# Kernel tuning notes

Measured on AMD Instinct MI355X. Metric: run time of the kernel, lower is better.

Reference implementation:

```python
import jax, jax.numpy as jnp
import numpy as np

N = 50000
F_IN = 256
H1, D1 = 8, 8            # conv1: 8 heads x 8 dims, concat -> 64
H2, C = 8, 16            # conv2: 8 heads x num_classes, concat -> 128
NEG_SLOPE = 0.2


def setup_inputs() -> dict:
    key = jax.random.key(0)
    ks = jax.random.split(key, 10)
    x = jax.random.normal(ks[0], (N, F_IN), dtype=jnp.float32)
    edge_index = jax.random.randint(ks[1], (2, 800000), 0, N, dtype=jnp.int64)
    s1 = 1.0 / np.sqrt(F_IN)
    s2 = 1.0 / np.sqrt(H1 * D1)
    return {
        "x": x,
        "edge_index": edge_index,
        "W1": jax.random.normal(ks[2], (F_IN, H1 * D1), dtype=jnp.float32) * s1,
        "a1_src": jax.random.normal(ks[3], (H1, D1), dtype=jnp.float32) * s2,
        "a1_dst": jax.random.normal(ks[4], (H1, D1), dtype=jnp.float32) * s2,
        "b1": jnp.zeros((H1 * D1,), dtype=jnp.float32),
        "W2": jax.random.normal(ks[5], (H1 * D1, H2 * C), dtype=jnp.float32) * s2,
        "a2_src": jax.random.normal(ks[6], (H2, C), dtype=jnp.float32) * (1.0 / np.sqrt(C)),
        "a2_dst": jax.random.normal(ks[7], (H2, C), dtype=jnp.float32) * (1.0 / np.sqrt(C)),
        "b2": jnp.zeros((H2 * C,), dtype=jnp.float32),
    }


def _add_self_loops(edge_index, n):
    loops = jnp.arange(n, dtype=edge_index.dtype)
    return jnp.concatenate([edge_index, jnp.stack([loops, loops])], axis=1)


def _gat_conv(x, src, dst, W, a_src, a_dst, b, heads, out_dim, n):
    # xw: [N, H, O]
    xw = (x @ W).reshape(n, heads, out_dim)
    al_src = jnp.einsum("nho,ho->nh", xw, a_src)  # [N, H]
    al_dst = jnp.einsum("nho,ho->nh", xw, a_dst)
    e = jax.nn.leaky_relu(al_src[src] + al_dst[dst], NEG_SLOPE)  # [E, H]
    # segment softmax over edges sharing a destination node
    e_max = jax.ops.segment_max(e, dst, num_segments=n)
    e_exp = jnp.exp(e - e_max[dst])
    denom = jax.ops.segment_sum(e_exp, dst, num_segments=n)
    alpha = e_exp / (denom[dst] + 1e-16)                          # [E, H]
    msg = xw[src] * alpha[:, :, None]                              # [E, H, O]
    out = jax.ops.segment_sum(msg, dst, num_segments=n)           # [N, H, O]
    return out.reshape(n, heads * out_dim) + b, alpha


def reference(x, edge_index, W1, a1_src, a1_dst, b1, W2, a2_src, a2_dst, b2):
    ei = _add_self_loops(edge_index, N)
    src, dst = ei[0], ei[1]
    # dropout is a no-op at inference (training=False)
    h1, alpha1 = _gat_conv(x, src, dst, W1, a1_src, a1_dst, b1, H1, D1, N)
    h1 = jax.nn.elu(h1)
    h2, _ = _gat_conv(h1, src, dst, W2, a2_src, a2_dst, b2, H2, C, N)
    logp = jax.nn.log_softmax(h2, axis=1)
    return logp, alpha1
```

## Files before the change

### kernel.cpp

```cpp
#include <hip/hip_runtime.h>

#define N_NODES 50000
#define N_EDGES 800000
#define N_TOT   850000
#define NEG 0.2f
#define ELLW 64

#define G1_TILES 782
#define G2_TILES 782

#define NBIN   250
#define NPBIN  200
#define BKBLK  200
#define EPBK   4000
#define BCAP   32
#define OCAP   4096

__device__ __forceinline__ float leaky(float x) { return x > 0.f ? x : NEG * x; }

__device__ __forceinline__ unsigned bf16pk(float a, float b) {
  unsigned ua = __float_as_uint(a), ub = __float_as_uint(b);
  ua = (ua + 0x7FFFu + ((ua >> 16) & 1u)) >> 16;
  ub = (ub + 0x7FFFu + ((ub >> 16) & 1u)) >> 16;
  return ua | (ub << 16);
}
__device__ __forceinline__ float blo(unsigned u) { return __uint_as_float(u << 16); }
__device__ __forceinline__ float bhi(unsigned u) { return __uint_as_float(u & 0xFFFF0000u); }
__device__ __forceinline__ float bh2f(unsigned short h) { return __uint_as_float(((unsigned)h) << 16); }

__global__ __launch_bounds__(256) void bin_gemm1_k(const float* __restrict__ x,
    const float* __restrict__ W1, const float* __restrict__ a1sv, const float* __restrict__ a1dv,
    unsigned short* __restrict__ xw1h, float* __restrict__ al1s, float* __restrict__ a1dd,
    const int* __restrict__ srcA, const int* __restrict__ dstA,
    unsigned* __restrict__ slots, unsigned short* __restrict__ bcnt2,
    unsigned* __restrict__ ofl, int* __restrict__ ofc)
{
  __shared__ __align__(16) char smem[33024];
  const int t = threadIdx.x;
  if (blockIdx.x < BKBLK) {
    unsigned (*buf)[BCAP] = (unsigned(*)[BCAP])smem;
    int* bc = (int*)(smem + 32000);
    for (int k = t; k < NBIN; k += 256) bc[k] = 0;
    __syncthreads();
    const int e0 = blockIdx.x * EPBK;
#pragma unroll
    for (int j = 0; j < 4; ++j) {
      int i4 = j * 256 + t;
      if (i4 < EPBK / 4) {
        int4 s4 = ((const int4*)(srcA + e0))[i4];
        int4 d4 = ((const int4*)(dstA + e0))[i4];
        int dd[4] = {d4.x, d4.y, d4.z, d4.w};
        int ss[4] = {s4.x, s4.y, s4.z, s4.w};
#pragma unroll
        for (int q = 0; q < 4; ++q) {
          int bin = dd[q] / NPBIN;
          unsigned rec = (unsigned)dd[q] | ((unsigned)ss[q] << 16);
          int p = atomicAdd(&bc[bin], 1);
          if (p < BCAP) buf[bin][p] = rec;
          else { int g = atomicAdd(ofc, 1); if (g < OCAP) ofl[g] = rec; }
        }
      }
    }
    __syncthreads();
    const int wv = t >> 6, ln = t & 63;
    for (int b = wv; b < NBIN; b += 4) {
      int c = bc[b]; if (c > BCAP) c = BCAP;
      if (ln == 0) bcnt2[(size_t)b * BKBLK + blockIdx.x] = (unsigned short)c;
      if (ln < c) slots[((size_t)b * BKBLK + blockIdx.x) * BCAP + ln] = buf[b][ln];
    }
    return;
  }
  float* xs  = (float*)smem;
  float* wsm = (float*)(smem + 8192);
  const int tx = t & 15, ty = t >> 4;
  const int n0 = (blockIdx.x - BKBLK) * 64;
  const int nl = t >> 2;
  const int ks = (t & 3) * 8;
  const int wk = t >> 3;
  const int wc = (t & 7) * 8;
  int gn = n0 + nl; if (gn >= N_NODES) gn = N_NODES - 1;
  const float* xrowb = x + (size_t)gn * 256 + ks;

  float acc[4][4];
#pragma unroll
  for (int r = 0; r < 4; ++r)
#pragma unroll
    for (int i = 0; i < 4; ++i) acc[r][i] = 0.f;

  float4 xv0, xv1, wv0, wv1;
  {
    const float4* xp = (const float4*)xrowb;
    xv0 = xp[0]; xv1 = xp[1];
    const float* wrow = W1 + (size_t)wk * 64 + wc;
    wv0 = ((const float4*)wrow)[0];
    wv1 = ((const float4*)wrow)[1];
  }
  for (int kc = 0; kc < 8; ++kc) {
    __syncthreads();
    xs[(ks + 0) * 64 + nl] = xv0.x;  xs[(ks + 1) * 64 + nl] = xv0.y;
    xs[(ks + 2) * 64 + nl] = xv0.z;  xs[(ks + 3) * 64 + nl] = xv0.w;
    xs[(ks + 4) * 64 + nl] = xv1.x;  xs[(ks + 5) * 64 + nl] = xv1.y;
    xs[(ks + 6) * 64 + nl] = xv1.z;  xs[(ks + 7) * 64 + nl] = xv1.w;
    ((float4*)&wsm[wk * 64 + wc])[0] = wv0;
    ((float4*)&wsm[wk * 64 + wc])[1] = wv1;
    __syncthreads();
    if (kc < 7) {
      const int kb = (kc + 1) * 32;
      const float4* xp = (const float4*)(xrowb + kb);
      xv0 = xp[0]; xv1 = xp[1];
      const float* wrow = W1 + (size_t)(kb + wk) * 64 + wc;
      wv0 = ((const float4*)wrow)[0];
      wv1 = ((const float4*)wrow)[1];
    }
#pragma unroll 4
    for (int k = 0; k < 32; ++k) {
      float4 xa = *(const float4*)&xs[k * 64 + ty * 4];
      float4 wv = *(const float4*)&wsm[k * 64 + tx * 4];
      float xn[4]; *(float4*)xn = xa;
      float wn[4]; *(float4*)wn = wv;
#pragma unroll
      for (int r = 0; r < 4; ++r)
#pragma unroll
        for (int i = 0; i < 4; ++i) acc[r][i] += xn[r] * wn[i];
    }
  }
  float cs[4], cd[4];
#pragma unroll
  for (int i = 0; i < 4; ++i) { cs[i] = a1sv[tx * 4 + i]; cd[i] = a1dv[tx * 4 + i]; }
#pragma unroll
  for (int r = 0; r < 4; ++r) {
    int n = n0 + ty * 4 + r;
    if (n >= N_NODES) break;
    uint2 pk;
    pk.x = bf16pk(acc[r][0], acc[r][1]);
    pk.y = bf16pk(acc[r][2], acc[r][3]);
    *(uint2*)(xw1h + (size_t)n * 64 + tx * 4) = pk;
    float ps = acc[r][0] * cs[0] + acc[r][1] * cs[1] + acc[r][2] * cs[2] + acc[r][3] * cs[3];
    float pd = acc[r][0] * cd[0] + acc[r][1] * cd[1] + acc[r][2] * cd[2] + acc[r][3] * cd[3];
    ps += __shfl_xor(ps, 1);
    pd += __shfl_xor(pd, 1);
    if ((tx & 1) == 0) {
      al1s[n * 8 + (tx >> 1)] = ps;
      a1dd[n * 16 + (tx >> 1)] = pd;
    }
  }
}

__global__ __launch_bounds__(256) void ell_k(const unsigned* __restrict__ slots,
    const unsigned short* __restrict__ bcnt2, const unsigned* __restrict__ ofl,
    const int* __restrict__ ofc, int* __restrict__ cnt, unsigned short* __restrict__ ell)
{
  __shared__ unsigned short ell_lds[NPBIN * ELLW];
  __shared__ int cnt_lds[NPBIN];
  const int t = threadIdx.x;
  const int b = blockIdx.x;
  for (int k = t; k < NPBIN; k += 256) cnt_lds[k] = 0;
  __syncthreads();
  if (t < BKBLK) {
    int c = bcnt2[(size_t)b * BKBLK + t];
    const uint4* sp4 = (const uint4*)(slots + ((size_t)b * BKBLK + t) * BCAP);
    uint4 R[8];
#pragma unroll
    for (int q = 0; q < 8; ++q) R[q] = sp4[q];
#pragma unroll
    for (int j = 0; j < BCAP; ++j) {
      if (j < c) {
        unsigned rec = ((const unsigned*)R)[j];
        int row = (int)(rec & 0xFFFFu) - b * NPBIN;
        int p = atomicAdd(&cnt_lds[row], 1);
        if (p < ELLW) ell_lds[row * ELLW + p] = (unsigned short)(rec >> 16);
      }
    }
  }
  __syncthreads();
  int oc = *ofc; if (oc > OCAP) oc = OCAP;
  for (int i = t; i < oc; i += 256) {
    unsigned rec = ofl[i];
    int d = rec & 0xFFFFu;
    if (d >= b * NPBIN && d < (b + 1) * NPBIN) {
      int p = atomicAdd(&cnt_lds[d - b * NPBIN], 1);
      if (p < ELLW) ell_lds[(d - b * NPBIN) * ELLW + p] = (unsigned short)(rec >> 16);
    }
  }
  __syncthreads();
  const uint4* s4 = (const uint4*)ell_lds;
  uint4* d4 = (uint4*)(ell + (size_t)b * NPBIN * ELLW);
  for (int i = t; i < NPBIN * ELLW / 8; i += 256) d4[i] = s4[i];
  for (int k = t; k < NPBIN; k += 256) cnt[b * NPBIN + k] = cnt_lds[k];
}

__global__ __launch_bounds__(256) void agg1_k(const unsigned short* __restrict__ xw1h,
    const float* __restrict__ al1s, float* __restrict__ a1dd,
    const int* __restrict__ cnt, const unsigned short* __restrict__ ell,
    const float* __restrict__ b1, float* __restrict__ h1)
{
  const unsigned lane = threadIdx.x & 63;
  const int n = blockIdx.x * 4 + (threadIdx.x >> 6);
  if (n >= N_NODES) return;
  const unsigned h = lane >> 3;
  const float ad = a1dd[n * 16 + h];
  float ws = __expf(leaky(al1s[n * 8 + h] + ad));
  float den0 = ws, den1 = 0.f;
  float acc0 = ws * bh2f(xw1h[((unsigned)n << 6) | lane]), acc1 = 0.f;
  int num = cnt[n]; if (num > ELLW) num = ELLW;
  const uint4* cp = (const uint4*)(ell + (size_t)n * ELLW);
  int i = 0;
  for (; i + 16 <= num; i += 16) {
    uint4 A = cp[i >> 3], B = cp[(i >> 3) + 1];
    unsigned s0 = A.x & 0xFFFFu, s1 = A.x >> 16, s2 = A.y & 0xFFFFu, s3 = A.y >> 16;
    unsigned s4 = A.z & 0xFFFFu, s5 = A.z >> 16, s6 = A.w & 0xFFFFu, s7 = A.w >> 16;
    unsigned s8 = B.x & 0xFFFFu, s9 = B.x >> 16, sA = B.y & 0xFFFFu, sB = B.y >> 16;
    unsigned sC = B.z & 0xFFFFu, sD = B.z >> 16, sE = B.w & 0xFFFFu, sF = B.w >> 16;
    float l0 = al1s[(s0 << 3) + h], l1 = al1s[(s1 << 3) + h];
    float l2 = al1s[(s2 << 3) + h], l3 = al1s[(s3 << 3) + h];
    float l4 = al1s[(s4 << 3) + h], l5 = al1s[(s5 << 3) + h];
    float l6 = al1s[(s6 << 3) + h], l7 = al1s[(s7 << 3) + h];
    float l8 = al1s[(s8 << 3) + h], l9 = al1s[(s9 << 3) + h];
    float lA = al1s[(sA << 3) + h], lB = al1s[(sB << 3) + h];
    float lC = al1s[(sC << 3) + h], lD = al1s[(sD << 3) + h];
    float lE = al1s[(sE << 3) + h], lF = al1s[(sF << 3) + h];
    float v0 = bh2f(xw1h[(s0 << 6) | lane]), v1 = bh2f(xw1h[(s1 << 6) | lane]);
    float v2 = bh2f(xw1h[(s2 << 6) | lane]), v3 = bh2f(xw1h[(s3 << 6) | lane]);
    float v4 = bh2f(xw1h[(s4 << 6) | lane]), v5 = bh2f(xw1h[(s5 << 6) | lane]);
    float v6 = bh2f(xw1h[(s6 << 6) | lane]), v7 = bh2f(xw1h[(s7 << 6) | lane]);
    float v8 = bh2f(xw1h[(s8 << 6) | lane]), v9 = bh2f(xw1h[(s9 << 6) | lane]);
    float vA = bh2f(xw1h[(sA << 6) | lane]), vB = bh2f(xw1h[(sB << 6) | lane]);
    float vC = bh2f(xw1h[(sC << 6) | lane]), vD = bh2f(xw1h[(sD << 6) | lane]);
    float vE = bh2f(xw1h[(sE << 6) | lane]), vF = bh2f(xw1h[(sF << 6) | lane]);
    float w0 = __expf(leaky(l0 + ad)), w1 = __expf(leaky(l1 + ad));
    float w2 = __expf(leaky(l2 + ad)), w3 = __expf(leaky(l3 + ad));
    float w4 = __expf(leaky(l4 + ad)), w5 = __expf(leaky(l5 + ad));
    float w6 = __expf(leaky(l6 + ad)), w7 = __expf(leaky(l7 + ad));
    float w8 = __expf(leaky(l8 + ad)), w9 = __expf(leaky(l9 + ad));
    float wA = __expf(leaky(lA + ad)), wB = __expf(leaky(lB + ad));
    float wC = __expf(leaky(lC + ad)), wD = __expf(leaky(lD + ad));
    float wE = __expf(leaky(lE + ad)), wF = __expf(leaky(lF + ad));
    acc0 += w0 * v0; acc1 += w1 * v1; acc0 += w2 * v2; acc1 += w3 * v3;
    acc0 += w4 * v4; acc1 += w5 * v5; acc0 += w6 * v6; acc1 += w7 * v7;
    acc0 += w8 * v8; acc1 += w9 * v9; acc0 += wA * vA; acc1 += wB * vB;
    acc0 += wC * vC; acc1 += wD * vD; acc0 += wE * vE; acc1 += wF * vF;
    den0 += w0 + w2 + w4 + w6 + w8 + wA + wC + wE;
    den1 += w1 + w3 + w5 + w7 + w9 + wB + wD + wF;
  }
  for (; i + 4 <= num; i += 4) {
    uint2 A = *(const uint2*)(ell + (size_t)n * ELLW + i);
    unsigned s0 = A.x & 0xFFFFu, s1 = A.x >> 16, s2 = A.y & 0xFFFFu, s3 = A.y >> 16;
    float l0 = al1s[(s0 << 3) + h], l1 = al1s[(s1 << 3) + h];
    float l2 = al1s[(s2 << 3) + h], l3 = al1s[(s3 << 3) + h];
    float v0 = bh2f(xw1h[(s0 << 6) | lane]), v1 = bh2f(xw1h[(s1 << 6) | lane]);
    float v2 = bh2f(xw1h[(s2 << 6) | lane]), v3 = bh2f(xw1h[(s3 << 6) | lane]);
    float w0 = __expf(leaky(l0 + ad)), w1 = __expf(leaky(l1 + ad));
    float w2 = __expf(leaky(l2 + ad)), w3 = __expf(leaky(l3 + ad));
    acc0 += w0 * v0; acc1 += w1 * v1; acc0 += w2 * v2; acc1 += w3 * v3;
    den0 += w0 + w2; den1 += w1 + w3;
  }
  for (; i < num; ++i) {
    unsigned s = ell[(size_t)n * ELLW + i];
    float w = __expf(leaky(al1s[(s << 3) + h] + ad));
    acc0 += w * bh2f(xw1h[(s << 6) | lane]);
    den0 += w;
  }
  float den = den0 + den1, acc = acc0 + acc1;
  if ((lane & 7) == 0) a1dd[n * 16 + 8 + h] = den;
  float o = acc / (den + 1e-16f) + b1[lane];
  h1[(size_t)n * 64 + lane] = o > 0.f ? o : (__expf(o) - 1.f);
}

__global__ __launch_bounds__(256) void gemm2_alpha_k(const float* __restrict__ h1,
    const float* __restrict__ W2, const float* __restrict__ a2sv, const float* __restrict__ a2dv,
    unsigned* __restrict__ xw2b, float* __restrict__ al2s, float* __restrict__ al2d,
    const int* __restrict__ srcA, const int* __restrict__ dstA,
    const float* __restrict__ al1s, const float* __restrict__ a1dd,
    float* __restrict__ alpha_out)
{
  __shared__ float xs[64 * 64];
  __shared__ float wsm[64 * 128];
  if (blockIdx.x >= G2_TILES) {
    int e = (blockIdx.x - G2_TILES) * 256 + threadIdx.x;
    if (e >= N_TOT) return;
    int s, d;
    if (e < N_EDGES) { s = srcA[e]; d = dstA[e]; }
    else             { s = d = e - N_EDGES; }
    float4 as0 = ((const float4*)(al1s + s * 8))[0];
    float4 as1 = ((const float4*)(al1s + s * 8))[1];
    const float4* dd = (const float4*)(a1dd + d * 16);
    float4 ad0 = dd[0];
    float4 ad1 = dd[1];
    float4 dn0 = dd[2];
    float4 dn1 = dd[3];
    float4 o0, o1;
    o0.x = __expf(leaky(as0.x + ad0.x)) / (dn0.x + 1e-16f);
    o0.y = __expf(leaky(as0.y + ad0.y)) / (dn0.y + 1e-16f);
    o0.z = __expf(leaky(as0.z + ad0.z)) / (dn0.z + 1e-16f);
    o0.w = __expf(leaky(as0.w + ad0.w)) / (dn0.w + 1e-16f);
    o1.x = __expf(leaky(as1.x + ad1.x)) / (dn1.x + 1e-16f);
    o1.y = __expf(leaky(as1.y + ad1.y)) / (dn1.y + 1e-16f);
    o1.z = __expf(leaky(as1.z + ad1.z)) / (dn1.z + 1e-16f);
    o1.w = __expf(leaky(as1.w + ad1.w)) / (dn1.w + 1e-16f);
    ((float4*)(alpha_out + (size_t)e * 8))[0] = o0;
    ((float4*)(alpha_out + (size_t)e * 8))[1] = o1;
    return;
  }
  const int t = threadIdx.x;
  const int tx = t & 15, ty = t >> 4;
  const int n0 = blockIdx.x * 64;
  {
    const int nl = t >> 2;
    const int ks = (t & 3) * 16;
    int gn = n0 + nl; if (gn >= N_NODES) gn = N_NODES - 1;
    const float4* hp = (const float4*)(h1 + (size_t)gn * 64 + ks);
#pragma unroll
    for (int j = 0; j < 4; ++j) {
      float4 v = hp[j];
      xs[(ks + 4 * j + 0) * 64 + nl] = v.x;
      xs[(ks + 4 * j + 1) * 64 + nl] = v.y;
      xs[(ks + 4 * j + 2) * 64 + nl] = v.z;
      xs[(ks + 4 * j + 3) * 64 + nl] = v.w;
    }
    const int wk = t >> 2;
    const int wc = (t & 3) * 32;
    const float4* wp = (const float4*)(W2 + (size_t)wk * 128 + wc);
    float4* wd = (float4*)&wsm[wk * 128 + wc];
#pragma unroll
    for (int j = 0; j < 8; ++j) wd[j] = wp[j];
  }
  __syncthreads();
  float acc[4][8];
#pragma unroll
  for (int r = 0; r < 4; ++r)
#pragma unroll
    for (int i = 0; i < 8; ++i) acc[r][i] = 0.f;
#pragma unroll 4
  for (int k = 0; k < 64; ++k) {
    float4 xa = *(const float4*)&xs[k * 64 + ty * 4];
    float4 wa = *(const float4*)&wsm[k * 128 + tx * 8];
    float4 wb = *(const float4*)&wsm[k * 128 + tx * 8 + 4];
    float xn[4]; *(float4*)xn = xa;
    float wn[8]; *(float4*)&wn[0] = wa; *(float4*)&wn[4] = wb;
#pragma unroll
    for (int r = 0; r < 4; ++r)
#pragma unroll
      for (int i = 0; i < 8; ++i) acc[r][i] += xn[r] * wn[i];
  }
  float cs[8], cd[8];
#pragma unroll
  for (int i = 0; i < 8; ++i) { cs[i] = a2sv[tx * 8 + i]; cd[i] = a2dv[tx * 8 + i]; }
#pragma unroll
  for (int r = 0; r < 4; ++r) {
    int n = n0 + ty * 4 + r;
    if (n >= N_NODES) break;
    uint4 pk;
    pk.x = bf16pk(acc[r][0], acc[r][1]);
    pk.y = bf16pk(acc[r][2], acc[r][3]);
    pk.z = bf16pk(acc[r][4], acc[r][5]);
    pk.w = bf16pk(acc[r][6], acc[r][7]);
    *(uint4*)(xw2b + (size_t)n * 64 + tx * 4) = pk;
    float ps = 0.f, pd = 0.f;
#pragma unroll
    for (int i = 0; i < 8; ++i) { ps += acc[r][i] * cs[i]; pd += acc[r][i] * cd[i]; }
    ps += __shfl_xor(ps, 1);
    pd += __shfl_xor(pd, 1);
    if ((tx & 1) == 0) {
      al2s[n * 8 + (tx >> 1)] = ps;
      al2d[n * 8 + (tx >> 1)] = pd;
    }
  }
}

__global__ __launch_bounds__(256) void agg2_k(const unsigned* __restrict__ xw2b,
    const float* __restrict__ al2s, const float* __restrict__ al2d,
    const int* __restrict__ cnt, const unsigned short* __restrict__ ell,
    const float* __restrict__ b2, float* __restrict__ logp)
{
  const unsigned lane = threadIdx.x & 63;
  const int n = blockIdx.x * 4 + (threadIdx.x >> 6);
  if (n >= N_NODES) return;
  const unsigned h = lane >> 3;
  const float ad = al2d[n * 8 + h];
  float ws = __expf(leaky(al2s[n * 8 + h] + ad));
  unsigned su = xw2b[((unsigned)n << 6) | lane];
  float den0 = ws, den1 = 0.f;
  float ax0 = ws * blo(su), ay0 = ws * bhi(su), ax1 = 0.f, ay1 = 0.f;
  int num = cnt[n]; if (num > ELLW) num = ELLW;
  const uint4* cp = (const uint4*)(ell + (size_t)n * ELLW);
  int i = 0;
  for (; i + 16 <= num; i += 16) {
    uint4 A = cp[i >> 3], B = cp[(i >> 3) + 1];
    unsigned s0 = A.x & 0xFFFFu, s1 = A.x >> 16, s2 = A.y & 0xFFFFu, s3 = A.y >> 16;
    unsigned s4 = A.z & 0xFFFFu, s5 = A.z >> 16, s6 = A.w & 0xFFFFu, s7 = A.w >> 16;
    unsigned s8 = B.x & 0xFFFFu, s9 = B.x >> 16, sA = B.y & 0xFFFFu, sB = B.y >> 16;
    unsigned sC = B.z & 0xFFFFu, sD = B.z >> 16, sE = B.w & 0xFFFFu, sF = B.w >> 16;
    float l0 = al2s[(s0 << 3) + h], l1 = al2s[(s1 << 3) + h];
    float l2 = al2s[(s2 << 3) + h], l3 = al2s[(s3 << 3) + h];
    float l4 = al2s[(s4 << 3) + h], l5 = al2s[(s5 << 3) + h];
    float l6 = al2s[(s6 << 3) + h], l7 = al2s[(s7 << 3) + h];
    float l8 = al2s[(s8 << 3) + h], l9 = al2s[(s9 << 3) + h];
    float lA = al2s[(sA << 3) + h], lB = al2s[(sB << 3) + h];
    float lC = al2s[(sC << 3) + h], lD = al2s[(sD << 3) + h];
    float lE = al2s[(sE << 3) + h], lF = al2s[(sF << 3) + h];
    unsigned u0 = xw2b[(s0 << 6) | lane], u1 = xw2b[(s1 << 6) | lane];
    unsigned u2 = xw2b[(s2 << 6) | lane], u3 = xw2b[(s3 << 6) | lane];
    unsigned u4 = xw2b[(s4 << 6) | lane], u5 = xw2b[(s5 << 6) | lane];
    unsigned u6 = xw2b[(s6 << 6) | lane], u7 = xw2b[(s7 << 6) | lane];
    unsigned u8 = xw2b[(s8 << 6) | lane], u9 = xw2b[(s9 << 6) | lane];
    unsigned uA = xw2b[(sA << 6) | lane], uB = xw2b[(sB << 6) | lane];
    unsigned uC = xw2b[(sC << 6) | lane], uD = xw2b[(sD << 6) | lane];
    unsigned uE = xw2b[(sE << 6) | lane], uF = xw2b[(sF << 6) | lane];
    float w0 = __expf(leaky(l0 + ad)), w1 = __expf(leaky(l1 + ad));
    float w2 = __expf(leaky(l2 + ad)), w3 = __expf(leaky(l3 + ad));
    float w4 = __expf(leaky(l4 + ad)), w5 = __expf(leaky(l5 + ad));
    float w6 = __expf(leaky(l6 + ad)), w7 = __expf(leaky(l7 + ad));
    float w8 = __expf(leaky(l8 + ad)), w9 = __expf(leaky(l9 + ad));
    float wA = __expf(leaky(lA + ad)), wB = __expf(leaky(lB + ad));
    float wC = __expf(leaky(lC + ad)), wD = __expf(leaky(lD + ad));
    float wE = __expf(leaky(lE + ad)), wF = __expf(leaky(lF + ad));
    ax0 += w0 * blo(u0); ay0 += w0 * bhi(u0);
    ax1 += w1 * blo(u1); ay1 += w1 * bhi(u1);
    ax0 += w2 * blo(u2); ay0 += w2 * bhi(u2);
    ax1 += w3 * blo(u3); ay1 += w3 * bhi(u3);
    ax0 += w4 * blo(u4); ay0 += w4 * bhi(u4);
    ax1 += w5 * blo(u5); ay1 += w5 * bhi(u5);
    ax0 += w6 * blo(u6); ay0 += w6 * bhi(u6);
    ax1 += w7 * blo(u7); ay1 += w7 * bhi(u7);
    ax0 += w8 * blo(u8); ay0 += w8 * bhi(u8);
    ax1 += w9 * blo(u9); ay1 += w9 * bhi(u9);
    ax0 += wA * blo(uA); ay0 += wA * bhi(uA);
    ax1 += wB * blo(uB); ay1 += wB * bhi(uB);
    ax0 += wC * blo(uC); ay0 += wC * bhi(uC);
    ax1 += wD * blo(uD); ay1 += wD * bhi(uD);
    ax0 += wE * blo(uE); ay0 += wE * bhi(uE);
    ax1 += wF * blo(uF); ay1 += wF * bhi(uF);
    den0 += w0 + w2 + w4 + w6 + w8 + wA + wC + wE;
    den1 += w1 + w3 + w5 + w7 + w9 + wB + wD + wF;
  }
  for (; i + 4 <= num; i += 4) {
    uint2 A = *(const uint2*)(ell + (size_t)n * ELLW + i);
    unsigned s0 = A.x & 0xFFFFu, s1 = A.x >> 16, s2 = A.y & 0xFFFFu, s3 = A.y >> 16;
    float l0 = al2s[(s0 << 3) + h], l1 = al2s[(s1 << 3) + h];
    float l2 = al2s[(s2 << 3) + h], l3 = al2s[(s3 << 3) + h];
    unsigned u0 = xw2b[(s0 << 6) | lane], u1 = xw2b[(s1 << 6) | lane];
    unsigned u2 = xw2b[(s2 << 6) | lane], u3 = xw2b[(s3 << 6) | lane];
    float w0 = __expf(leaky(l0 + ad)), w1 = __expf(leaky(l1 + ad));
    float w2 = __expf(leaky(l2 + ad)), w3 = __expf(leaky(l3 + ad));
    ax0 += w0 * blo(u0); ay0 += w0 * bhi(u0);
    ax1 += w1 * blo(u1); ay1 += w1 * bhi(u1);
    ax0 += w2 * blo(u2); ay0 += w2 * bhi(u2);
    ax1 += w3 * blo(u3); ay1 += w3 * bhi(u3);
    den0 += w0 + w2; den1 += w1 + w3;
  }
  for (; i < num; ++i) {
    unsigned s = ell[(size_t)n * ELLW + i];
    float w = __expf(leaky(al2s[(s << 3) + h] + ad));
    unsigned u = xw2b[(s << 6) | lane];
    ax0 += w * blo(u); ay0 += w * bhi(u); den0 += w;
  }
  float inv = 1.f / (den0 + den1 + 1e-16f);
  float o0 = (ax0 + ax1) * inv + b2[2 * lane];
  float o1 = (ay0 + ay1) * inv + b2[2 * lane + 1];
  float mx = fmaxf(o0, o1);
#pragma unroll
  for (int off = 1; off < 64; off <<= 1) mx = fmaxf(mx, __shfl_xor(mx, off));
  float se = __expf(o0 - mx) + __expf(o1 - mx);
#pragma unroll
  for (int off = 1; off < 64; off <<= 1) se += __shfl_xor(se, off);
  float lse = mx + __logf(se);
  float2 o; o.x = o0 - lse; o.y = o1 - lse;
  ((float2*)logp)[(size_t)n * 64 + lane] = o;
}

extern "C" void kernel_launch(void* const* d_in, const int* in_sizes, int n_in,
                              void* d_out, int out_size, void* d_ws, size_t ws_size,
                              hipStream_t stream)
{
  const float* x   = (const float*)d_in[0];
  const int*   ei  = (const int*)d_in[1];
  const float* W1  = (const float*)d_in[2];
  const float* a1s = (const float*)d_in[3];
  const float* a1d = (const float*)d_in[4];
  const float* b1  = (const float*)d_in[5];
  const float* W2  = (const float*)d_in[6];
  const float* a2s = (const float*)d_in[7];
  const float* a2d = (const float*)d_in[8];
  const float* b2  = (const float*)d_in[9];
  const int* srcA = ei;
  const int* dstA = ei + N_EDGES;

  char* ws = (char*)d_ws;
  unsigned short* xw1h = (unsigned short*)ws;            ws += (size_t)N_NODES * 64 * 2;
  float* h1    = (float*)ws;  ws += (size_t)N_NODES * 64 * 4;
  unsigned* xw2b = (unsigned*)ws; ws += (size_t)N_NODES * 64 * 4;
  float* al1s_ = (float*)ws;  ws += (size_t)N_NODES * 8 * 4;
  float* a1dd_ = (float*)ws;  ws += (size_t)N_NODES * 16 * 4;
  float* al2s_ = (float*)ws;  ws += (size_t)N_NODES * 8 * 4;
  float* al2d_ = (float*)ws;  ws += (size_t)N_NODES * 8 * 4;
  int* cnt    = (int*)ws;     ws += (size_t)N_NODES * 4;
  unsigned short* ell = (unsigned short*)ws; ws += (size_t)N_NODES * ELLW * 2;
  unsigned* slots = (unsigned*)ws; ws += (size_t)NBIN * BKBLK * BCAP * 4;
  unsigned short* bcnt2 = (unsigned short*)ws; ws += (size_t)NBIN * BKBLK * 2;
  unsigned* ofl = (unsigned*)ws; ws += (size_t)OCAP * 4;
  int* ofc = (int*)ws; ws += 16;

  float* logp      = (float*)d_out;
  float* alpha_out = logp + (size_t)N_NODES * 128;

  hipMemsetAsync(ofc, 0, sizeof(int), stream);

  bin_gemm1_k<<<BKBLK + G1_TILES, 256, 0, stream>>>(
      x, W1, a1s, a1d, xw1h, al1s_, a1dd_, srcA, dstA, slots, bcnt2, ofl, ofc);
  ell_k<<<NBIN, 256, 0, stream>>>(slots, bcnt2, ofl, ofc, cnt, ell);
  agg1_k<<<(N_NODES + 3) / 4, 256, 0, stream>>>(xw1h, al1s_, a1dd_, cnt, ell, b1, h1);
  gemm2_alpha_k<<<G2_TILES + (N_TOT + 255) / 256, 256, 0, stream>>>(
      h1, W2, a2s, a2d, xw2b, al2s_, al2d_, srcA, dstA, al1s_, a1dd_, alpha_out);
  agg2_k<<<(N_NODES + 3) / 4, 256, 0, stream>>>(xw2b, al2s_, al2d_, cnt, ell, b2, logp);
}
```

Baseline: 167.7 us.

## Compute edge attention weights once per lane and broadcast via wave shuffles

In both aggregation kernels each wavefront used to compute the exp/leaky attention weight redundantly in every lane of a head group, which meant 8 identical al_s gathers and exps per edge-head. Now each of the 64 lanes computes one (edge, head) weight for a batch of 8 edges and the weights are redistributed with __shfl. This also halves the main-loop unroll from 16 to 8 edges. Leaky ReLU becomes a fmax. The change cuts redundant transcendental and gather work but adds 8 cross-lane shuffles per batch and shrinks the memory-level parallelism per iteration.

```diff
diff --git a/kernel.cpp b/kernel.cpp
--- a/kernel.cpp
+++ b/kernel.cpp
@@ -16,7 +16,7 @@
 #define BCAP   32
 #define OCAP   4096
 
-__device__ __forceinline__ float leaky(float x) { return x > 0.f ? x : NEG * x; }
+__device__ __forceinline__ float leaky(float x) { return fmaxf(x, NEG * x); }
 
 __device__ __forceinline__ unsigned bf16pk(float a, float b) {
   unsigned ua = __float_as_uint(a), ub = __float_as_uint(b);
@@ -27,6 +27,11 @@
 __device__ __forceinline__ float blo(unsigned u) { return __uint_as_float(u << 16); }
 __device__ __forceinline__ float bhi(unsigned u) { return __uint_as_float(u & 0xFFFF0000u); }
 __device__ __forceinline__ float bh2f(unsigned short h) { return __uint_as_float(((unsigned)h) << 16); }
+
+__device__ __forceinline__ unsigned sel8(uint4 A, unsigned e) {
+  unsigned w = (e & 4) ? ((e & 2) ? A.w : A.z) : ((e & 2) ? A.y : A.x);
+  return (e & 1) ? (w >> 16) : (w & 0xFFFFu);
+}
 
 __global__ __launch_bounds__(256) void bin_gemm1_k(const float* __restrict__ x,
     const float* __restrict__ W1, const float* __restrict__ a1sv, const float* __restrict__ a1dv,
@@ -198,59 +203,45 @@
   const int n = blockIdx.x * 4 + (threadIdx.x >> 6);
   if (n >= N_NODES) return;
   const unsigned h = lane >> 3;
+  const unsigned hw = lane & 7;
+  const unsigned ew = lane >> 3;
   const float ad = a1dd[n * 16 + h];
+  const float adH = __shfl(ad, (int)(hw << 3));
   float ws = __expf(leaky(al1s[n * 8 + h] + ad));
   float den0 = ws, den1 = 0.f;
-  float acc0 = ws * bh2f(xw1h[((unsigned)n << 6) | lane]), acc1 = 0.f;
+  float acc0 = ws * bh2f(xw1h[(size_t)n * 64 + lane]), acc1 = 0.f;
   int num = cnt[n]; if (num > ELLW) num = ELLW;
   const uint4* cp = (const uint4*)(ell + (size_t)n * ELLW);
   int i = 0;
-  for (; i + 16 <= num; i += 16) {
-    uint4 A = cp[i >> 3], B = cp[(i >> 3) + 1];
-    unsigned s0 = A.x & 0xFFFFu, s1 = A.x >> 16, s2 = A.y & 0xFFFFu, s3 = A.y >> 16;
-    unsigned s4 = A.z & 0xFFFFu, s5 = A.z >> 16, s6 = A.w & 0xFFFFu, s7 = A.w >> 16;
-    unsigned s8 = B.x & 0xFFFFu, s9 = B.x >> 16, sA = B.y & 0xFFFFu, sB = B.y >> 16;
-    unsigned sC = B.z & 0xFFFFu, sD = B.z >> 16, sE = B.w & 0xFFFFu, sF = B.w >> 16;
-    float l0 = al1s[(s0 << 3) + h], l1 = al1s[(s1 << 3) + h];
-    float l2 = al1s[(s2 << 3) + h], l3 = al1s[(s3 << 3) + h];
-    float l4 = al1s[(s4 << 3) + h], l5 = al1s[(s5 << 3) + h];
-    float l6 = al1s[(s6 << 3) + h], l7 = al1s[(s7 << 3) + h];
-    float l8 = al1s[(s8 << 3) + h], l9 = al1s[(s9 << 3) + h];
-    float lA = al1s[(sA << 3) + h], lB = al1s[(sB << 3) + h];
-    float lC = al1s[(sC << 3) + h], lD = al1s[(sD << 3) + h];
-    float lE = al1s[(sE << 3) + h], lF = al1s[(sF << 3) + h];
+  for (; i + 8 <= num; i += 8) {
+    uint4 A = cp[i >> 3];
+    unsigned s0 = A.x & 0xFFFFu, s1 = A.x >> 16;
+    unsigned s2 = A.y & 0xFFFFu, s3 = A.y >> 16;
+    unsigned s4 = A.z & 0xFFFFu, s5 = A.z >> 16;
+    unsigned s6 = A.w & 0xFFFFu, s7 = A.w >> 16;
+    unsigned ssel = sel8(A, ew);
+    float wv = __expf(leaky(al1s[(ssel << 3) + hw] + adH));
     float v0 = bh2f(xw1h[(s0 << 6) | lane]), v1 = bh2f(xw1h[(s1 << 6) | lane]);
     float v2 = bh2f(xw1h[(s2 << 6) | lane]), v3 = bh2f(xw1h[(s3 << 6) | lane]);
     float v4 = bh2f(xw1h[(s4 << 6) | lane]), v5 = bh2f(xw1h[(s5 << 6) | lane]);
     float v6 = bh2f(xw1h[(s6 << 6) | lane]), v7 = bh2f(xw1h[(s7 << 6) | lane]);
-    float v8 = bh2f(xw1h[(s8 << 6) | lane]), v9 = bh2f(xw1h[(s9 << 6) | lane]);
-    float vA = bh2f(xw1h[(sA << 6) | lane]), vB = bh2f(xw1h[(sB << 6) | lane]);
-    float vC = bh2f(xw1h[(sC << 6) | lane]), vD = bh2f(xw1h[(sD << 6) | lane]);
-    float vE = bh2f(xw1h[(sE << 6) | lane]), vF = bh2f(xw1h[(sF << 6) | lane]);
-    float w0 = __expf(leaky(l0 + ad)), w1 = __expf(leaky(l1 + ad));
-    float w2 = __expf(leaky(l2 + ad)), w3 = __expf(leaky(l3 + ad));
-    float w4 = __expf(leaky(l4 + ad)), w5 = __expf(leaky(l5 + ad));
-    float w6 = __expf(leaky(l6 + ad)), w7 = __expf(leaky(l7 + ad));
-    float w8 = __expf(leaky(l8 + ad)), w9 = __expf(leaky(l9 + ad));
-    float wA = __expf(leaky(lA + ad)), wB = __expf(leaky(lB + ad));
-    float wC = __expf(leaky(lC + ad)), wD = __expf(leaky(lD + ad));
-    float wE = __expf(leaky(lE + ad)), wF = __expf(leaky(lF + ad));
+    float w0 = __shfl(wv, (int)(0 * 8 + h)), w1 = __shfl(wv, (int)(1 * 8 + h));
+    float w2 = __shfl(wv, (int)(2 * 8 + h)), w3 = __shfl(wv, (int)(3 * 8 + h));
+    float w4 = __shfl(wv, (int)(4 * 8 + h)), w5 = __shfl(wv, (int)(5 * 8 + h));
+    float w6 = __shfl(wv, (int)(6 * 8 + h)), w7 = __shfl(wv, (int)(7 * 8 + h));
     acc0 += w0 * v0; acc1 += w1 * v1; acc0 += w2 * v2; acc1 += w3 * v3;
     acc0 += w4 * v4; acc1 += w5 * v5; acc0 += w6 * v6; acc1 += w7 * v7;
-    acc0 += w8 * v8; acc1 += w9 * v9; acc0 += wA * vA; acc1 += wB * vB;
-    acc0 += wC * vC; acc1 += wD * vD; acc0 += wE * vE; acc1 += wF * vF;
-    den0 += w0 + w2 + w4 + w6 + w8 + wA + wC + wE;
-    den1 += w1 + w3 + w5 + w7 + w9 + wB + wD + wF;
+    den0 += w0 + w2 + w4 + w6; den1 += w1 + w3 + w5 + w7;
   }
   for (; i + 4 <= num; i += 4) {
     uint2 A = *(const uint2*)(ell + (size_t)n * ELLW + i);
     unsigned s0 = A.x & 0xFFFFu, s1 = A.x >> 16, s2 = A.y & 0xFFFFu, s3 = A.y >> 16;
-    float l0 = al1s[(s0 << 3) + h], l1 = al1s[(s1 << 3) + h];
-    float l2 = al1s[(s2 << 3) + h], l3 = al1s[(s3 << 3) + h];
+    float l0 = al1s[(s0 << 3) + h] + ad, l1 = al1s[(s1 << 3) + h] + ad;
+    float l2 = al1s[(s2 << 3) + h] + ad, l3 = al1s[(s3 << 3) + h] + ad;
     float v0 = bh2f(xw1h[(s0 << 6) | lane]), v1 = bh2f(xw1h[(s1 << 6) | lane]);
     float v2 = bh2f(xw1h[(s2 << 6) | lane]), v3 = bh2f(xw1h[(s3 << 6) | lane]);
-    float w0 = __expf(leaky(l0 + ad)), w1 = __expf(leaky(l1 + ad));
-    float w2 = __expf(leaky(l2 + ad)), w3 = __expf(leaky(l3 + ad));
+    float w0 = __expf(leaky(l0)), w1 = __expf(leaky(l1));
+    float w2 = __expf(leaky(l2)), w3 = __expf(leaky(l3));
     acc0 += w0 * v0; acc1 += w1 * v1; acc0 += w2 * v2; acc1 += w3 * v3;
     den0 += w0 + w2; den1 += w1 + w3;
   }
@@ -376,44 +367,33 @@
   const int n = blockIdx.x * 4 + (threadIdx.x >> 6);
   if (n >= N_NODES) return;
   const unsigned h = lane >> 3;
+  const unsigned hw = lane & 7;
+  const unsigned ew = lane >> 3;
   const float ad = al2d[n * 8 + h];
+  const float adH = __shfl(ad, (int)(hw << 3));
   float ws = __expf(leaky(al2s[n * 8 + h] + ad));
-  unsigned su = xw2b[((unsigned)n << 6) | lane];
+  unsigned su = xw2b[(size_t)n * 64 + lane];
   float den0 = ws, den1 = 0.f;
   float ax0 = ws * blo(su), ay0 = ws * bhi(su), ax1 = 0.f, ay1 = 0.f;
   int num = cnt[n]; if (num > ELLW) num = ELLW;
   const uint4* cp = (const uint4*)(ell + (size_t)n * ELLW);
   int i = 0;
-  for (; i + 16 <= num; i += 16) {
-    uint4 A = cp[i >> 3], B = cp[(i >> 3) + 1];
-    unsigned s0 = A.x & 0xFFFFu, s1 = A.x >> 16, s2 = A.y & 0xFFFFu, s3 = A.y >> 16;
-    unsigned s4 = A.z & 0xFFFFu, s5 = A.z >> 16, s6 = A.w & 0xFFFFu, s7 = A.w >> 16;
-    unsigned s8 = B.x & 0xFFFFu, s9 = B.x >> 16, sA = B.y & 0xFFFFu, sB = B.y >> 16;
-    unsigned sC = B.z & 0xFFFFu, sD = B.z >> 16, sE = B.w & 0xFFFFu, sF = B.w >> 16;
-    float l0 = al2s[(s0 << 3) + h], l1 = al2s[(s1 << 3) + h];
-    float l2 = al2s[(s2 << 3) + h], l3 = al2s[(s3 << 3) + h];
-    float l4 = al2s[(s4 << 3) + h], l5 = al2s[(s5 << 3) + h];
-    float l6 = al2s[(s6 << 3) + h], l7 = al2s[(s7 << 3) + h];
-    float l8 = al2s[(s8 << 3) + h], l9 = al2s[(s9 << 3) + h];
-    float lA = al2s[(sA << 3) + h], lB = al2s[(sB << 3) + h];
-    float lC = al2s[(sC << 3) + h], lD = al2s[(sD << 3) + h];
-    float lE = al2s[(sE << 3) + h], lF = al2s[(sF << 3) + h];
+  for (; i + 8 <= num; i += 8) {
+    uint4 A = cp[i >> 3];
+    unsigned s0 = A.x & 0xFFFFu, s1 = A.x >> 16;
+    unsigned s2 = A.y & 0xFFFFu, s3 = A.y >> 16;
+    unsigned s4 = A.z & 0xFFFFu, s5 = A.z >> 16;
+    unsigned s6 = A.w & 0xFFFFu, s7 = A.w >> 16;
+    unsigned ssel = sel8(A, ew);
+    float wv = __expf(leaky(al2s[(ssel << 3) + hw] + adH));
     unsigned u0 = xw2b[(s0 << 6) | lane], u1 = xw2b[(s1 << 6) | lane];
     unsigned u2 = xw2b[(s2 << 6) | lane], u3 = xw2b[(s3 << 6) | lane];
     unsigned u4 = xw2b[(s4 << 6) | lane], u5 = xw2b[(s5 << 6) | lane];
     unsigned u6 = xw2b[(s6 << 6) | lane], u7 = xw2b[(s7 << 6) | lane];
-    unsigned u8 = xw2b[(s8 << 6) | lane], u9 = xw2b[(s9 << 6) | lane];
-    unsigned uA = xw2b[(sA << 6) | lane], uB = xw2b[(sB << 6) | lane];
-    unsigned uC = xw2b[(sC << 6) | lane], uD = xw2b[(sD << 6) | lane];
-    unsigned uE = xw2b[(sE << 6) | lane], uF = xw2b[(sF << 6) | lane];
-    float w0 = __expf(leaky(l0 + ad)), w1 = __expf(leaky(l1 + ad));
-    float w2 = __expf(leaky(l2 + ad)), w3 = __expf(leaky(l3 + ad));
-    float w4 = __expf(leaky(l4 + ad)), w5 = __expf(leaky(l5 + ad));
-    float w6 = __expf(leaky(l6 + ad)), w7 = __expf(leaky(l7 + ad));
-    float w8 = __expf(leaky(l8 + ad)), w9 = __expf(leaky(l9 + ad));
-    float wA = __expf(leaky(lA + ad)), wB = __expf(leaky(lB + ad));
-    float wC = __expf(leaky(lC + ad)), wD = __expf(leaky(lD + ad));
-    float wE = __expf(leaky(lE + ad)), wF = __expf(leaky(lF + ad));
+    float w0 = __shfl(wv, (int)(0 * 8 + h)), w1 = __shfl(wv, (int)(1 * 8 + h));
+    float w2 = __shfl(wv, (int)(2 * 8 + h)), w3 = __shfl(wv, (int)(3 * 8 + h));
+    float w4 = __shfl(wv, (int)(4 * 8 + h)), w5 = __shfl(wv, (int)(5 * 8 + h));
+    float w6 = __shfl(wv, (int)(6 * 8 + h)), w7 = __shfl(wv, (int)(7 * 8 + h));
     ax0 += w0 * blo(u0); ay0 += w0 * bhi(u0);
     ax1 += w1 * blo(u1); ay1 += w1 * bhi(u1);
     ax0 += w2 * blo(u2); ay0 += w2 * bhi(u2);
@@ -422,26 +402,17 @@
     ax1 += w5 * blo(u5); ay1 += w5 * bhi(u5);
     ax0 += w6 * blo(u6); ay0 += w6 * bhi(u6);
     ax1 += w7 * blo(u7); ay1 += w7 * bhi(u7);
-    ax0 += w8 * blo(u8); ay0 += w8 * bhi(u8);
-    ax1 += w9 * blo(u9); ay1 += w9 * bhi(u9);
-    ax0 += wA * blo(uA); ay0 += wA * bhi(uA);
-    ax1 += wB * blo(uB); ay1 += wB * bhi(uB);
-    ax0 += wC * blo(uC); ay0 += wC * bhi(uC);
-    ax1 += wD * blo(uD); ay1 += wD * bhi(uD);
-    ax0 += wE * blo(uE); ay0 += wE * bhi(uE);
-    ax1 += wF * blo(uF); ay1 += wF * bhi(uF);
-    den0 += w0 + w2 + w4 + w6 + w8 + wA + wC + wE;
-    den1 += w1 + w3 + w5 + w7 + w9 + wB + wD + wF;
+    den0 += w0 + w2 + w4 + w6; den1 += w1 + w3 + w5 + w7;
   }
   for (; i + 4 <= num; i += 4) {
     uint2 A = *(const uint2*)(ell + (size_t)n * ELLW + i);
     unsigned s0 = A.x & 0xFFFFu, s1 = A.x >> 16, s2 = A.y & 0xFFFFu, s3 = A.y >> 16;
-    float l0 = al2s[(s0 << 3) + h], l1 = al2s[(s1 << 3) + h];
-    float l2 = al2s[(s2 << 3) + h], l3 = al2s[(s3 << 3) + h];
+    float l0 = al2s[(s0 << 3) + h] + ad, l1 = al2s[(s1 << 3) + h] + ad;
+    float l2 = al2s[(s2 << 3) + h] + ad, l3 = al2s[(s3 << 3) + h] + ad;
     unsigned u0 = xw2b[(s0 << 6) | lane], u1 = xw2b[(s1 << 6) | lane];
     unsigned u2 = xw2b[(s2 << 6) | lane], u3 = xw2b[(s3 << 6) | lane];
-    float w0 = __expf(leaky(l0 + ad)), w1 = __expf(leaky(l1 + ad));
-    float w2 = __expf(leaky(l2 + ad)), w3 = __expf(leaky(l3 + ad));
+    float w0 = __expf(leaky(l0)), w1 = __expf(leaky(l1));
+    float w2 = __expf(leaky(l2)), w3 = __expf(leaky(l3));
     ax0 += w0 * blo(u0); ay0 += w0 * bhi(u0);
     ax1 += w1 * blo(u1); ay1 += w1 * bhi(u1);
     ax0 += w2 * blo(u2); ay0 += w2 * bhi(u2);
```

Result: faster. 156.5 us (median of 2 runs) (-6.7%).
